# Kernel tuning notes

Hardware: AMD Instinct MI355X
Metric: run time of the kernel (lower is better)

Reference implementation:

```python
import jax, jax.numpy as jnp
import numpy as np

T = 2048       # tokens (flattened, single causal sequence)
HID = 2048     # hidden_size
H = 16         # num_heads
DN = 128       # qk_nope_head_dim
DR = 64        # qk_rope_head_dim
DV = 128       # v_head_dim
DQK = DN + DR  # 192
QLR = 1536     # q_lora_rank
KVLR = 512     # kv_lora_rank
THETA = 10000.0
EPS = 1e-6
SCALE = DQK ** -0.5


def rmsnorm(x, w):
    return x * jax.lax.rsqrt(jnp.mean(x * x, axis=-1, keepdims=True) + EPS) * w


def rope_interleaved(x, cos, sin):
    # is_neox_style=False: rotate interleaved even/odd pairs
    x1 = x[..., 0::2]
    x2 = x[..., 1::2]
    out = jnp.stack([x1 * cos - x2 * sin, x2 * cos + x1 * sin], axis=-1)
    return out.reshape(x.shape)


def setup_inputs() -> dict:
    key = jax.random.key(0)
    ks = jax.random.split(key, 8)
    s = 0.02
    return {
        "positions": jnp.arange(T, dtype=jnp.int32),
        "hidden_states": jax.random.normal(ks[0], (T, HID), jnp.float32),
        "w_q_a": jax.random.normal(ks[1], (HID, QLR), jnp.float32) * s,
        "q_a_ln_w": jnp.ones((QLR,), jnp.float32),
        "w_q_b": jax.random.normal(ks[2], (QLR, H * DQK), jnp.float32) * s,
        "w_kv_a": jax.random.normal(ks[3], (HID, KVLR + DR), jnp.float32) * s,
        "kv_a_ln_w": jnp.ones((KVLR,), jnp.float32),
        "w_kv_b": jax.random.normal(ks[4], (KVLR, H * (DN + DV)), jnp.float32) * s,
        "w_o": jax.random.normal(ks[5], (H * DV, HID), jnp.float32) * s,
    }


def reference(positions, hidden_states, w_q_a, q_a_ln_w, w_q_b, w_kv_a,
              kv_a_ln_w, w_kv_b, w_o):
    t = hidden_states.shape[0]
    # --- Q low-rank path ---
    q = rmsnorm(hidden_states @ w_q_a, q_a_ln_w) @ w_q_b          # [T, H*DQK]
    q = q.reshape(t, H, DQK)
    q_nope, q_pe = q[..., :DN], q[..., DN:]
    # --- KV latent path ---
    latent = hidden_states @ w_kv_a                                # [T, KVLR+DR]
    kv_a = rmsnorm(latent[:, :KVLR], kv_a_ln_w)
    kv = (kv_a @ w_kv_b).reshape(t, H, DN + DV)
    k_nope, v = kv[..., :DN], kv[..., DN:]
    k_pe = latent[:, None, KVLR:]                                  # [T, 1, DR]
    # --- partial RoPE (non-neox, interleaved) ---
    inv_freq = 1.0 / (THETA ** (jnp.arange(0, DR, 2, dtype=jnp.float32) / DR))
    ang = positions.astype(jnp.float32)[:, None] * inv_freq        # [T, DR/2]
    cos = jnp.cos(ang)[:, None, :]
    sin = jnp.sin(ang)[:, None, :]
    q_pe = rope_interleaved(q_pe, cos, sin)
    k_pe = rope_interleaved(k_pe, cos, sin)
    q = jnp.concatenate([q_nope, q_pe], axis=-1)                   # [T, H, DQK]
    k = jnp.concatenate([k_nope, jnp.broadcast_to(k_pe, (t, H, DR))], axis=-1)
    # --- causal attention (V zero-padded to DQK then sliced == using V directly) ---
    scores = jnp.einsum("thd,shd->hts", q, k) * SCALE              # [H, T, T]
    causal = positions[None, :, None] >= positions[None, None, :]
    scores = jnp.where(causal, scores, jnp.finfo(scores.dtype).min)
    probs = jax.nn.softmax(scores, axis=-1)
    attn = jnp.einsum("hts,shd->thd", probs, v)                    # [T, H, DV]
    return attn.reshape(t, H * DV) @ w_o                           # [T, HID]
```

## Files before the change

kernel.cpp:

```cpp
#include <hip/hip_runtime.h>
#include <hip/hip_bf16.h>

#define T_ 2048
#define SCALE_ 0.07216878364870322f

typedef __bf16 bf16x8 __attribute__((ext_vector_type(8)));
typedef float f32x4 __attribute__((ext_vector_type(4)));
typedef float f32x16 __attribute__((ext_vector_type(16)));

__device__ inline bf16x8 load8f(const float* p) {
    const float4* f = reinterpret_cast<const float4*>(p);
    float4 a = f[0], b = f[1];
    bf16x8 r;
    r[0] = (__bf16)a.x; r[1] = (__bf16)a.y; r[2] = (__bf16)a.z; r[3] = (__bf16)a.w;
    r[4] = (__bf16)b.x; r[5] = (__bf16)b.y; r[6] = (__bf16)b.z; r[7] = (__bf16)b.w;
    return r;
}

__device__ inline void gld_lds16(const void* g, void* l) {
    __builtin_amdgcn_global_load_lds((const __attribute__((address_space(1))) void*)g,
                                     (__attribute__((address_space(3))) void*)l, 16, 0, 0);
}

__global__ __launch_bounds__(256) void cvt_bf16(const float* __restrict__ in,
                                                __bf16* __restrict__ out, int n8)
{
    int i = blockIdx.x * 256 + threadIdx.x;
    if (i < n8)
        *reinterpret_cast<bf16x8*>(out + (size_t)i * 8) = load8f(in + (size_t)i * 8);
}

__global__ __launch_bounds__(256) void transpose_cvt(
    const float* __restrict__ W, __bf16* __restrict__ Wt, int K, int N)
{
    __shared__ __bf16 tl[64][72];
    const int k0 = blockIdx.x * 64, n0 = blockIdx.y * 64;
    const int tid = threadIdx.x;
    const bool in = n0 < N;
    #pragma unroll
    for (int it = 0; it < 2; ++it) {
        int chunk = tid + it * 256;
        int r = chunk >> 3;
        int c8 = (chunk & 7) * 8;
        float4 a = {0,0,0,0}, b = {0,0,0,0};
        if (in) {
            const float* p = W + (size_t)(k0 + r) * N + n0 + c8;
            a = *reinterpret_cast<const float4*>(p);
            b = *reinterpret_cast<const float4*>(p + 4);
        }
        tl[c8+0][r] = (__bf16)a.x; tl[c8+1][r] = (__bf16)a.y;
        tl[c8+2][r] = (__bf16)a.z; tl[c8+3][r] = (__bf16)a.w;
        tl[c8+4][r] = (__bf16)b.x; tl[c8+5][r] = (__bf16)b.y;
        tl[c8+6][r] = (__bf16)b.z; tl[c8+7][r] = (__bf16)b.w;
    }
    __syncthreads();
    #pragma unroll
    for (int it = 0; it < 2; ++it) {
        int chunk = tid + it * 256;
        int n = chunk >> 3;
        int k8 = (chunk & 7) * 8;
        bf16x8 v = *reinterpret_cast<const bf16x8*>(&tl[n][k8]);
        *reinterpret_cast<bf16x8*>(Wt + (size_t)(n0 + n) * K + k0 + k8) = v;
    }
}

template <typename TC>
__device__ __forceinline__ void gemm_body(
    const __bf16* __restrict__ A, const __bf16* __restrict__ Bt,
    TC* __restrict__ C, int K, int Nstore, int ldc, int m0, int n0,
    __bf16* As, __bf16* Bs)
{
    const int tid = threadIdx.x, lane = tid & 63, wid = tid >> 6;
    const int l15 = lane & 15, lg = lane >> 4;
    const int wr = (wid >> 1) * 64, wc = (wid & 1) * 64;

    const int srow = wid * 32 + (lane >> 3);
    const int scol = ((lane & 7) ^ (lane >> 3)) * 8;
    const __bf16* Ag = A  + (size_t)(m0 + srow) * K + scol;
    const __bf16* Bg = Bt + (size_t)(n0 + srow) * K + scol;
    const int lbase = wid * 4096;

    f32x4 acc[4][4] = {};

    {
        char* la = (char*)As + lbase;
        char* lb = (char*)Bs + lbase;
        #pragma unroll
        for (int i = 0; i < 4; ++i) {
            gld_lds16(Ag + (size_t)i * 8 * K, la + i * 1024);
            gld_lds16(Bg + (size_t)i * 8 * K, lb + i * 1024);
        }
    }
    __syncthreads();

    int cur = 0;
    for (int k0 = 0; k0 < K; k0 += 64) {
        if (k0 + 64 < K) {
            char* la = (char*)As + (cur ^ 1) * 16384 + lbase;
            char* lb = (char*)Bs + (cur ^ 1) * 16384 + lbase;
            #pragma unroll
            for (int i = 0; i < 4; ++i) {
                gld_lds16(Ag + (size_t)i * 8 * K + k0 + 64, la + i * 1024);
                gld_lds16(Bg + (size_t)i * 8 * K + k0 + 64, lb + i * 1024);
            }
        }

        bf16x8 af[4][2], bf[4][2];
        #pragma unroll
        for (int i = 0; i < 4; ++i) {
            const int Ra = wr + i * 16 + l15;
            const int Rb = wc + i * 16 + l15;
            const int ca = (lg ^ (Ra & 7)) * 16;
            const int cb = (lg ^ (Rb & 7)) * 16;
            const char* pa = (const char*)As + cur * 16384 + Ra * 128;
            const char* pb = (const char*)Bs + cur * 16384 + Rb * 128;
            af[i][0] = *reinterpret_cast<const bf16x8*>(pa + ca);
            af[i][1] = *reinterpret_cast<const bf16x8*>(pa + (ca ^ 64));
            bf[i][0] = *reinterpret_cast<const bf16x8*>(pb + cb);
            bf[i][1] = *reinterpret_cast<const bf16x8*>(pb + (cb ^ 64));
        }
        #pragma unroll
        for (int h = 0; h < 2; ++h)
            #pragma unroll
            for (int i = 0; i < 4; ++i)
                #pragma unroll
                for (int j = 0; j < 4; ++j)
                    acc[i][j] = __builtin_amdgcn_mfma_f32_16x16x32_bf16(af[i][h], bf[j][h], acc[i][j], 0, 0, 0);

        __syncthreads();
        cur ^= 1;
    }

    #pragma unroll
    for (int i = 0; i < 4; ++i)
        #pragma unroll
        for (int j = 0; j < 4; ++j)
            #pragma unroll
            for (int e = 0; e < 4; ++e) {
                int r = m0 + wr + i * 16 + lg * 4 + e;
                int c = n0 + wc + j * 16 + l15;
                if (c < Nstore)
                    C[(size_t)r * ldc + c] = (TC)acc[i][j][e];
            }
}

template <typename TC>
__global__ __launch_bounds__(256) void gemm_bt(
    const __bf16* __restrict__ A, const __bf16* __restrict__ Bt,
    TC* __restrict__ C, int M, int N, int K, int Nstore, int ldc)
{
    __shared__ __bf16 As[2 * 128 * 64];
    __shared__ __bf16 Bs[2 * 128 * 64];
    gemm_body<TC>(A, Bt, C, K, Nstore, ldc, blockIdx.x * 128, blockIdx.y * 128, As, Bs);
}

__global__ __launch_bounds__(256) void gemm_bt_pair(
    const __bf16* __restrict__ A0, const __bf16* __restrict__ B0, __bf16* __restrict__ C0,
    int N0, int K0, int nby0,
    const __bf16* __restrict__ A1, const __bf16* __restrict__ B1, __bf16* __restrict__ C1,
    int N1, int K1)
{
    __shared__ __bf16 As[2 * 128 * 64];
    __shared__ __bf16 Bs[2 * 128 * 64];
    if ((int)blockIdx.y < nby0)
        gemm_body<__bf16>(A0, B0, C0, K0, N0, N0, blockIdx.x * 128, blockIdx.y * 128, As, Bs);
    else
        gemm_body<__bf16>(A1, B1, C1, K1, N1, N1, blockIdx.x * 128, (blockIdx.y - nby0) * 128, As, Bs);
}

__global__ __launch_bounds__(256) void rmsnorm_fused(
    const __bf16* __restrict__ qkv_a,
    const float* __restrict__ qw, const float* __restrict__ kw,
    __bf16* __restrict__ q_a_n, __bf16* __restrict__ kv_a_n)
{
    const int t = blockIdx.x, tid = threadIdx.x, wid = tid >> 6;
    const bool isq = tid < 192;
    const __bf16* src = qkv_a + (size_t)t * 2176 + (isq ? tid * 8 : 1536 + (tid - 192) * 8);
    float x[8];
    float ss = 0.f;
    bf16x8 v = *reinterpret_cast<const bf16x8*>(src);
    #pragma unroll
    for (int e = 0; e < 8; ++e) { x[e] = (float)v[e]; ss += x[e] * x[e]; }
    #pragma unroll
    for (int m = 1; m < 64; m <<= 1) ss += __shfl_xor(ss, m, 64);
    __shared__ float red[4];
    if ((tid & 63) == 0) red[wid] = ss;
    __syncthreads();
    float scale;
    const float* w;
    if (isq) {
        scale = rsqrtf((red[0] + red[1] + red[2]) / 1536.f + 1e-6f);
        w = qw + tid * 8;
    } else {
        scale = rsqrtf(red[3] / 512.f + 1e-6f);
        w = kw + (tid - 192) * 8;
    }
    float4 w0 = *reinterpret_cast<const float4*>(w);
    float4 w1 = *reinterpret_cast<const float4*>(w + 4);
    bf16x8 o;
    o[0] = (__bf16)(x[0] * scale * w0.x); o[1] = (__bf16)(x[1] * scale * w0.y);
    o[2] = (__bf16)(x[2] * scale * w0.z); o[3] = (__bf16)(x[3] * scale * w0.w);
    o[4] = (__bf16)(x[4] * scale * w1.x); o[5] = (__bf16)(x[5] * scale * w1.y);
    o[6] = (__bf16)(x[6] * scale * w1.z); o[7] = (__bf16)(x[7] * scale * w1.w);
    if (isq)
        *reinterpret_cast<bf16x8*>(q_a_n + (size_t)t * 1536 + tid * 8) = o;
    else
        *reinterpret_cast<bf16x8*>(kv_a_n + (size_t)t * 512 + (tid - 192) * 8) = o;
}

__global__ __launch_bounds__(256) void rope_kprep(
    const int* __restrict__ positions, __bf16* __restrict__ q,
    const __bf16* __restrict__ kv, const __bf16* __restrict__ qkv_a,
    __bf16* __restrict__ kh)
{
    const int t = blockIdx.x, tid = threadIdx.x;
    __shared__ float cs[32], sn[32];
    __shared__ __bf16 kpe[64];
    if (tid < 32) {
        float pos = (float)positions[t];
        float invf = powf(10000.f, -(float)tid / 32.f);
        float c = cosf(pos * invf), s = sinf(pos * invf);
        cs[tid] = c; sn[tid] = s;
        float x1 = (float)qkv_a[(size_t)t * 2176 + 2048 + 2 * tid];
        float x2 = (float)qkv_a[(size_t)t * 2176 + 2049 + 2 * tid];
        kpe[2 * tid]     = (__bf16)(x1 * c - x2 * s);
        kpe[2 * tid + 1] = (__bf16)(x2 * c + x1 * s);
    }
    __syncthreads();
    #pragma unroll
    for (int it = 0; it < 2; ++it) {
        int p = tid + it * 256;
        int h = p >> 5, i = p & 31;
        size_t base = (size_t)t * 3072 + h * 192 + 128 + 2 * i;
        float x1 = (float)q[base], x2 = (float)q[base + 1];
        q[base]     = (__bf16)(x1 * cs[i] - x2 * sn[i]);
        q[base + 1] = (__bf16)(x2 * cs[i] + x1 * sn[i]);
    }
    const int h = tid >> 4, c = tid & 15;
    const int sw = t & 7;
    bf16x8 v = *reinterpret_cast<const bf16x8*>(kv + (size_t)t * 4096 + h * 256 + c * 8);
    *reinterpret_cast<bf16x8*>(kh + ((size_t)h * T_ + t) * 192 + (c ^ sw) * 8) = v;
    if (c < 8) {
        bf16x8 p = *reinterpret_cast<const bf16x8*>(&kpe[c * 8]);
        *reinterpret_cast<bf16x8*>(kh + ((size_t)h * T_ + t) * 192 + 128 + (c ^ sw) * 8) = p;
    }
}

__global__ __launch_bounds__(256) void vtrans(
    const __bf16* __restrict__ kv, __bf16* __restrict__ vt)
{
    __shared__ __bf16 tile[128][72];
    const int t0 = blockIdx.x * 64;
    const int h  = blockIdx.y;
    const int tid = threadIdx.x;
    #pragma unroll
    for (int it = 0; it < 4; ++it) {
        int chunk = tid + it * 256;
        int r = chunk >> 4;
        int d8 = (chunk & 15) * 8;
        bf16x8 v = *reinterpret_cast<const bf16x8*>(kv + (size_t)(t0 + r) * 4096 + h * 256 + 128 + d8);
        #pragma unroll
        for (int e = 0; e < 8; ++e) tile[d8 + e][r] = v[e];
    }
    __syncthreads();
    #pragma unroll
    for (int it = 0; it < 4; ++it) {
        int chunk = tid + it * 256;
        int d = chunk >> 3;
        int t8 = (chunk & 7) * 8;
        bf16x8 v = *reinterpret_cast<const bf16x8*>(&tile[d][t8]);
        *reinterpret_cast<bf16x8*>(vt + ((size_t)h * 128 + d) * 2048 + t0 + t8) = v;
    }
}

__device__ inline unsigned pk2(float a, float b) {
    union { __bf16 h[2]; unsigned u; } z;
    z.h[0] = (__bf16)a; z.h[1] = (__bf16)b;
    return z.u;
}

union AttnSmem {
    char kstage[4][12288];
    struct {
        float mls[2][4][32];
        float linv[32];
        float obuf[32][129];
    } c;
};

__global__ __launch_bounds__(256, 2) void attn_flash(
    const __bf16* __restrict__ q, const __bf16* __restrict__ kh,
    const __bf16* __restrict__ vt, __bf16* __restrict__ attn)
{
    __shared__ AttnSmem sm;
    const int tid = threadIdx.x;
    const int lane = tid & 63, wid = tid >> 6;
    const int q31 = lane & 31, hi = lane >> 5;
    const int b = blockIdx.x;
    const int h = b & 15;
    const int qt = 63 - (b >> 4);
    const int q0 = qt * 32;
    const int ntile = qt + 1;

    const __bf16* Khh = kh + (size_t)h * T_ * 192;
    const __bf16* Vt  = vt + (size_t)h * 128 * T_;
    const __bf16* Qp  = q + (size_t)(q0 + q31) * 3072 + h * 192;

    bf16x8 aq[12];
    #pragma unroll
    for (int c = 0; c < 12; ++c)
        aq[c] = *reinterpret_cast<const bf16x8*>(Qp + c * 16 + hi * 8);

    f32x16 o[4] = {};
    float m_i = -1e30f, l_i = 0.f;

    char* kbuf = sm.kstage[wid];

    if (wid < ntile) {
        const __bf16* src = Khh + (size_t)(wid * 32) * 192 + lane * 8;
        #pragma unroll
        for (int i = 0; i < 12; ++i)
            gld_lds16(src + i * 512, kbuf + i * 1024);
    }

    for (int it = wid; it < ntile; it += 4) {
        asm volatile("s_waitcnt vmcnt(0)" ::: "memory");
        __builtin_amdgcn_sched_barrier(0);

        bf16x8 kc[12];
        #pragma unroll
        for (int c = 0; c < 12; ++c) {
            const int p = (2 * c + hi) ^ (q31 & 7);
            kc[c] = *reinterpret_cast<const bf16x8*>(kbuf + q31 * 384 + p * 16);
        }
        asm volatile("s_waitcnt lgkmcnt(0)" ::: "memory");
        __builtin_amdgcn_sched_barrier(0);

        const bool notlast = (it + 4 < ntile);
        if (notlast) {
            const __bf16* src = Khh + (size_t)((it + 4) * 32) * 192 + lane * 8;
            #pragma unroll
            for (int i = 0; i < 12; ++i)
                gld_lds16(src + i * 512, kbuf + i * 1024);
        }

        const int s0 = it * 32;
        bf16x8 vf[4][2];
        #pragma unroll
        for (int n = 0; n < 4; ++n)
            #pragma unroll
            for (int m = 0; m < 2; ++m)
                vf[n][m] = *reinterpret_cast<const bf16x8*>(
                    Vt + (size_t)(n * 32 + q31) * 2048 + s0 + (2 * m + hi) * 8);

        f32x16 sA = {}, sB = {};
        __builtin_amdgcn_s_setprio(1);
        #pragma unroll
        for (int c = 0; c < 12; c += 2) {
            sA = __builtin_amdgcn_mfma_f32_32x32x16_bf16(kc[c],     aq[c],     sA, 0, 0, 0);
            sB = __builtin_amdgcn_mfma_f32_32x32x16_bf16(kc[c + 1], aq[c + 1], sB, 0, 0, 0);
        }
        __builtin_amdgcn_s_setprio(0);

        float v[16];
        #pragma unroll
        for (int r = 0; r < 16; ++r) v[r] = (sA[r] + sB[r]) * SCALE_;
        if (it == qt) {
            #pragma unroll
            for (int r = 0; r < 16; ++r) {
                int crow = (r & 3) + 8 * (r >> 2) + 4 * hi;
                if (crow > q31) v[r] = -1e30f;
            }
        }
        float mx = v[0];
        #pragma unroll
        for (int r = 1; r < 16; ++r) mx = fmaxf(mx, v[r]);
        mx = fmaxf(mx, __shfl_xor(mx, 32, 64));
        const bool skip = __all(mx <= m_i);
        float mnew = fmaxf(m_i, mx);
        float fsc = skip ? 1.f : __expf(m_i - mnew);
        m_i = mnew;
        float ps = 0.f;
        #pragma unroll
        for (int r = 0; r < 16; ++r) { v[r] = __expf(v[r] - mnew); ps += v[r]; }
        ps += __shfl_xor(ps, 32, 64);
        l_i = l_i * fsc + ps;
        if (!skip) {
            #pragma unroll
            for (int n = 0; n < 4; ++n) o[n] *= fsc;
        }

        unsigned w[8], xw[8];
        #pragma unroll
        for (int i = 0; i < 8; ++i) w[i] = pk2(v[2 * i], v[2 * i + 1]);
        #pragma unroll
        for (int i = 0; i < 8; ++i) xw[i] = __shfl_xor(w[i], 32, 64);
        union { unsigned u[4]; bf16x8 v; } P0, P1;
        P0.u[0] = hi ? xw[2] : w[0]; P0.u[1] = hi ? xw[3] : w[1];
        P0.u[2] = hi ? w[2] : xw[0]; P0.u[3] = hi ? w[3] : xw[1];
        P1.u[0] = hi ? xw[6] : w[4]; P1.u[1] = hi ? xw[7] : w[5];
        P1.u[2] = hi ? w[6] : xw[4]; P1.u[3] = hi ? w[7] : xw[5];

        __builtin_amdgcn_s_setprio(1);
        #pragma unroll
        for (int n = 0; n < 4; ++n) {
            o[n] = __builtin_amdgcn_mfma_f32_32x32x16_bf16(vf[n][0], P0.v, o[n], 0, 0, 0);
            o[n] = __builtin_amdgcn_mfma_f32_32x32x16_bf16(vf[n][1], P1.v, o[n], 0, 0, 0);
        }
        __builtin_amdgcn_s_setprio(0);
    }

    __syncthreads();
    if (hi == 0) { sm.c.mls[0][wid][q31] = m_i; sm.c.mls[1][wid][q31] = l_i; }
    __syncthreads();
    float M = fmaxf(fmaxf(sm.c.mls[0][0][q31], sm.c.mls[0][1][q31]),
                    fmaxf(sm.c.mls[0][2][q31], sm.c.mls[0][3][q31]));
    float L = sm.c.mls[1][0][q31] * __expf(sm.c.mls[0][0][q31] - M)
            + sm.c.mls[1][1][q31] * __expf(sm.c.mls[0][1][q31] - M)
            + sm.c.mls[1][2][q31] * __expf(sm.c.mls[0][2][q31] - M)
            + sm.c.mls[1][3][q31] * __expf(sm.c.mls[0][3][q31] - M);
    float F = __expf(m_i - M);
    if (wid == 0 && hi == 0) sm.c.linv[q31] = 1.f / L;

    #pragma unroll
    for (int rd = 0; rd < 4; ++rd) {
        if (wid == rd) {
            if (rd == 0) {
                #pragma unroll
                for (int n = 0; n < 4; ++n)
                    #pragma unroll
                    for (int r = 0; r < 16; ++r) {
                        int d = (r & 3) + 8 * (r >> 2) + 4 * hi + 32 * n;
                        sm.c.obuf[q31][d] = F * o[n][r];
                    }
            } else {
                #pragma unroll
                for (int n = 0; n < 4; ++n)
                    #pragma unroll
                    for (int r = 0; r < 16; ++r) {
                        int d = (r & 3) + 8 * (r >> 2) + 4 * hi + 32 * n;
                        sm.c.obuf[q31][d] += F * o[n][r];
                    }
            }
        }
        __syncthreads();
    }

    #pragma unroll
    for (int it2 = 0; it2 < 2; ++it2) {
        int cidx = tid + it2 * 256;
        int row = cidx >> 4, c8 = (cidx & 15) * 8;
        float inv = sm.c.linv[row];
        bf16x8 vv;
        #pragma unroll
        for (int j = 0; j < 8; ++j)
            vv[j] = (__bf16)(sm.c.obuf[row][c8 + j] * inv);
        *reinterpret_cast<bf16x8*>(attn + (size_t)(q0 + row) * 2048 + h * 128 + c8) = vv;
    }
}

extern "C" void kernel_launch(void* const* d_in, const int* in_sizes, int n_in,
                              void* d_out, int out_size, void* d_ws, size_t ws_size,
                              hipStream_t stream)
{
    const int*   positions = (const int*)d_in[0];
    const float* hidden    = (const float*)d_in[1];
    const float* w_q_a     = (const float*)d_in[2];
    const float* q_a_ln_w  = (const float*)d_in[3];
    const float* w_q_b     = (const float*)d_in[4];
    const float* w_kv_a    = (const float*)d_in[5];
    const float* kv_a_ln_w = (const float*)d_in[6];
    const float* w_kv_b    = (const float*)d_in[7];
    const float* w_o       = (const float*)d_in[8];

    char* ws = (char*)d_ws;
    __bf16* hidden_bf = (__bf16*)(ws);
    __bf16* vt        = (__bf16*)(ws);
    __bf16* wbuf      = (__bf16*)(ws + 8388608);
    __bf16* qkv_a     = (__bf16*)(ws + 17825792);
    __bf16* attn      = (__bf16*)(ws + 17825792);
    __bf16* q_a_n     = (__bf16*)(ws + 26738688);
    __bf16* q         = (__bf16*)(ws + 33030144);
    __bf16* kv_a_n    = (__bf16*)(ws + 45613056);
    __bf16* kv        = (__bf16*)(ws + 47710208);
    __bf16* kh        = (__bf16*)(ws + 64487424);
    __bf16* wbuf2     = (__bf16*)(ws + 77070336);

    dim3 blk(256);
    cvt_bf16<<<dim3(2048), blk, 0, stream>>>(hidden, hidden_bf, 524288);

    transpose_cvt<<<dim3(32, 24), blk, 0, stream>>>(w_q_a, wbuf, 2048, 1536);
    transpose_cvt<<<dim3(32, 10), blk, 0, stream>>>(w_kv_a, wbuf + (size_t)1536 * 2048, 2048, 576);
    gemm_bt<__bf16><<<dim3(16, 17), blk, 0, stream>>>(hidden_bf, wbuf, qkv_a, 2048, 2176, 2048, 2112, 2176);
    rmsnorm_fused<<<dim3(2048), blk, 0, stream>>>(qkv_a, q_a_ln_w, kv_a_ln_w, q_a_n, kv_a_n);

    transpose_cvt<<<dim3(24, 48), blk, 0, stream>>>(w_q_b, wbuf, 1536, 3072);
    transpose_cvt<<<dim3(8, 64), blk, 0, stream>>>(w_kv_b, wbuf2, 512, 4096);
    gemm_bt_pair<<<dim3(16, 56), blk, 0, stream>>>(
        q_a_n, wbuf, q, 3072, 1536, 24,
        kv_a_n, wbuf2, kv, 4096, 512);

    rope_kprep<<<dim3(2048), blk, 0, stream>>>(positions, q, kv, qkv_a, kh);
    vtrans<<<dim3(32, 16), blk, 0, stream>>>(kv, vt);
    attn_flash<<<dim3(1024), dim3(256), 0, stream>>>(q, kh, vt, attn);

    transpose_cvt<<<dim3(32, 32), blk, 0, stream>>>(w_o, wbuf, 2048, 2048);
    gemm_bt<float><<<dim3(16, 16), blk, 0, stream>>>(attn, wbuf, (float*)d_out, 2048, 2048, 2048, 2048, 2048);
}
```

Measured before the change: 221.8 us.

## Process two K tiles per attention loop iteration with direct global K loads

Each wave now handles two key tiles per loop trip, tile it through the LDS-staged buffer and tile it+4 through direct global register loads of K issued before the first QK MFMA. The LDS prefetch now targets it+8. The aim is more memory-level parallelism and better latency hiding between the two tiles' loads and MFMAs. It costs more registers (a second K fragment and V fragment set), which may lower occupancy, and the second tile's K reads bypass LDS. The direct loads apply a swizzle based on the row index, which only matches the data if the K buffer in global memory is itself stored swizzled.

```diff
diff --git a/kernel.cpp b/kernel.cpp
--- a/kernel.cpp
+++ b/kernel.cpp
@@ -323,7 +323,10 @@
             gld_lds16(src + i * 512, kbuf + i * 1024);
     }
 
-    for (int it = wid; it < ntile; it += 4) {
+    for (int it = wid; it < ntile; it += 8) {
+        const int itB = it + 4;
+        const bool hasB = (itB < ntile);
+
         asm volatile("s_waitcnt vmcnt(0)" ::: "memory");
         __builtin_amdgcn_sched_barrier(0);
 
@@ -336,14 +339,6 @@
         asm volatile("s_waitcnt lgkmcnt(0)" ::: "memory");
         __builtin_amdgcn_sched_barrier(0);
 
-        const bool notlast = (it + 4 < ntile);
-        if (notlast) {
-            const __bf16* src = Khh + (size_t)((it + 4) * 32) * 192 + lane * 8;
-            #pragma unroll
-            for (int i = 0; i < 12; ++i)
-                gld_lds16(src + i * 512, kbuf + i * 1024);
-        }
-
         const int s0 = it * 32;
         bf16x8 vf[4][2];
         #pragma unroll
@@ -353,6 +348,24 @@
                 vf[n][m] = *reinterpret_cast<const bf16x8*>(
                     Vt + (size_t)(n * 32 + q31) * 2048 + s0 + (2 * m + hi) * 8);
 
+        if (it + 8 < ntile) {
+            const __bf16* src = Khh + (size_t)((it + 8) * 32) * 192 + lane * 8;
+            #pragma unroll
+            for (int i = 0; i < 12; ++i)
+                gld_lds16(src + i * 512, kbuf + i * 1024);
+        }
+
+        bf16x8 kb[12];
+        if (hasB) {
+            const __bf16* KgB = Khh + (size_t)(itB * 32 + q31) * 192;
+            const int swB = (itB * 32 + q31) & 7;
+            #pragma unroll
+            for (int c = 0; c < 12; ++c) {
+                const int p = (2 * c + hi) ^ swB;
+                kb[c] = *reinterpret_cast<const bf16x8*>(KgB + p * 8);
+            }
+        }
+
         f32x16 sA = {}, sB = {};
         __builtin_amdgcn_s_setprio(1);
         #pragma unroll
@@ -362,52 +375,121 @@
         }
         __builtin_amdgcn_s_setprio(0);
 
-        float v[16];
-        #pragma unroll
-        for (int r = 0; r < 16; ++r) v[r] = (sA[r] + sB[r]) * SCALE_;
-        if (it == qt) {
-            #pragma unroll
-            for (int r = 0; r < 16; ++r) {
-                int crow = (r & 3) + 8 * (r >> 2) + 4 * hi;
-                if (crow > q31) v[r] = -1e30f;
-            }
-        }
-        float mx = v[0];
-        #pragma unroll
-        for (int r = 1; r < 16; ++r) mx = fmaxf(mx, v[r]);
-        mx = fmaxf(mx, __shfl_xor(mx, 32, 64));
-        const bool skip = __all(mx <= m_i);
-        float mnew = fmaxf(m_i, mx);
-        float fsc = skip ? 1.f : __expf(m_i - mnew);
-        m_i = mnew;
-        float ps = 0.f;
-        #pragma unroll
-        for (int r = 0; r < 16; ++r) { v[r] = __expf(v[r] - mnew); ps += v[r]; }
-        ps += __shfl_xor(ps, 32, 64);
-        l_i = l_i * fsc + ps;
-        if (!skip) {
-            #pragma unroll
-            for (int n = 0; n < 4; ++n) o[n] *= fsc;
-        }
-
-        unsigned w[8], xw[8];
-        #pragma unroll
-        for (int i = 0; i < 8; ++i) w[i] = pk2(v[2 * i], v[2 * i + 1]);
-        #pragma unroll
-        for (int i = 0; i < 8; ++i) xw[i] = __shfl_xor(w[i], 32, 64);
-        union { unsigned u[4]; bf16x8 v; } P0, P1;
-        P0.u[0] = hi ? xw[2] : w[0]; P0.u[1] = hi ? xw[3] : w[1];
-        P0.u[2] = hi ? w[2] : xw[0]; P0.u[3] = hi ? w[3] : xw[1];
-        P1.u[0] = hi ? xw[6] : w[4]; P1.u[1] = hi ? xw[7] : w[5];
-        P1.u[2] = hi ? w[6] : xw[4]; P1.u[3] = hi ? w[7] : xw[5];
-
-        __builtin_amdgcn_s_setprio(1);
-        #pragma unroll
-        for (int n = 0; n < 4; ++n) {
-            o[n] = __builtin_amdgcn_mfma_f32_32x32x16_bf16(vf[n][0], P0.v, o[n], 0, 0, 0);
-            o[n] = __builtin_amdgcn_mfma_f32_32x32x16_bf16(vf[n][1], P1.v, o[n], 0, 0, 0);
-        }
-        __builtin_amdgcn_s_setprio(0);
+        {
+            float v[16];
+            #pragma unroll
+            for (int r = 0; r < 16; ++r) v[r] = (sA[r] + sB[r]) * SCALE_;
+            if (it == qt) {
+                #pragma unroll
+                for (int r = 0; r < 16; ++r) {
+                    int crow = (r & 3) + 8 * (r >> 2) + 4 * hi;
+                    if (crow > q31) v[r] = -1e30f;
+                }
+            }
+            float mx = v[0];
+            #pragma unroll
+            for (int r = 1; r < 16; ++r) mx = fmaxf(mx, v[r]);
+            mx = fmaxf(mx, __shfl_xor(mx, 32, 64));
+            const bool skip = __all(mx <= m_i);
+            float mnew = fmaxf(m_i, mx);
+            float fsc = skip ? 1.f : __expf(m_i - mnew);
+            m_i = mnew;
+            float ps = 0.f;
+            #pragma unroll
+            for (int r = 0; r < 16; ++r) { v[r] = __expf(v[r] - mnew); ps += v[r]; }
+            ps += __shfl_xor(ps, 32, 64);
+            l_i = l_i * fsc + ps;
+            if (!skip) {
+                #pragma unroll
+                for (int n = 0; n < 4; ++n) o[n] *= fsc;
+            }
+
+            unsigned w[8], xw[8];
+            #pragma unroll
+            for (int i = 0; i < 8; ++i) w[i] = pk2(v[2 * i], v[2 * i + 1]);
+            #pragma unroll
+            for (int i = 0; i < 8; ++i) xw[i] = __shfl_xor(w[i], 32, 64);
+            union { unsigned u[4]; bf16x8 v; } P0, P1;
+            P0.u[0] = hi ? xw[2] : w[0]; P0.u[1] = hi ? xw[3] : w[1];
+            P0.u[2] = hi ? w[2] : xw[0]; P0.u[3] = hi ? w[3] : xw[1];
+            P1.u[0] = hi ? xw[6] : w[4]; P1.u[1] = hi ? xw[7] : w[5];
+            P1.u[2] = hi ? w[6] : xw[4]; P1.u[3] = hi ? w[7] : xw[5];
+
+            __builtin_amdgcn_s_setprio(1);
+            #pragma unroll
+            for (int n = 0; n < 4; ++n) {
+                o[n] = __builtin_amdgcn_mfma_f32_32x32x16_bf16(vf[n][0], P0.v, o[n], 0, 0, 0);
+                o[n] = __builtin_amdgcn_mfma_f32_32x32x16_bf16(vf[n][1], P1.v, o[n], 0, 0, 0);
+            }
+            __builtin_amdgcn_s_setprio(0);
+        }
+
+        if (hasB) {
+            const int s0B = itB * 32;
+            bf16x8 vfB[4][2];
+            #pragma unroll
+            for (int n = 0; n < 4; ++n)
+                #pragma unroll
+                for (int m = 0; m < 2; ++m)
+                    vfB[n][m] = *reinterpret_cast<const bf16x8*>(
+                        Vt + (size_t)(n * 32 + q31) * 2048 + s0B + (2 * m + hi) * 8);
+
+            f32x16 tA = {}, tB = {};
+            __builtin_amdgcn_s_setprio(1);
+            #pragma unroll
+            for (int c = 0; c < 12; c += 2) {
+                tA = __builtin_amdgcn_mfma_f32_32x32x16_bf16(kb[c],     aq[c],     tA, 0, 0, 0);
+                tB = __builtin_amdgcn_mfma_f32_32x32x16_bf16(kb[c + 1], aq[c + 1], tB, 0, 0, 0);
+            }
+            __builtin_amdgcn_s_setprio(0);
+
+            float v[16];
+            #pragma unroll
+            for (int r = 0; r < 16; ++r) v[r] = (tA[r] + tB[r]) * SCALE_;
+            if (itB == qt) {
+                #pragma unroll
+                for (int r = 0; r < 16; ++r) {
+                    int crow = (r & 3) + 8 * (r >> 2) + 4 * hi;
+                    if (crow > q31) v[r] = -1e30f;
+                }
+            }
+            float mx = v[0];
+            #pragma unroll
+            for (int r = 1; r < 16; ++r) mx = fmaxf(mx, v[r]);
+            mx = fmaxf(mx, __shfl_xor(mx, 32, 64));
+            const bool skip = __all(mx <= m_i);
+            float mnew = fmaxf(m_i, mx);
+            float fsc = skip ? 1.f : __expf(m_i - mnew);
+            m_i = mnew;
+            float ps = 0.f;
+            #pragma unroll
+            for (int r = 0; r < 16; ++r) { v[r] = __expf(v[r] - mnew); ps += v[r]; }
+            ps += __shfl_xor(ps, 32, 64);
+            l_i = l_i * fsc + ps;
+            if (!skip) {
+                #pragma unroll
+                for (int n = 0; n < 4; ++n) o[n] *= fsc;
+            }
+
+            unsigned w[8], xw[8];
+            #pragma unroll
+            for (int i = 0; i < 8; ++i) w[i] = pk2(v[2 * i], v[2 * i + 1]);
+            #pragma unroll
+            for (int i = 0; i < 8; ++i) xw[i] = __shfl_xor(w[i], 32, 64);
+            union { unsigned u[4]; bf16x8 v; } P0, P1;
+            P0.u[0] = hi ? xw[2] : w[0]; P0.u[1] = hi ? xw[3] : w[1];
+            P0.u[2] = hi ? w[2] : xw[0]; P0.u[3] = hi ? w[3] : xw[1];
+            P1.u[0] = hi ? xw[6] : w[4]; P1.u[1] = hi ? xw[7] : w[5];
+            P1.u[2] = hi ? w[6] : xw[4]; P1.u[3] = hi ? w[7] : xw[5];
+
+            __builtin_amdgcn_s_setprio(1);
+            #pragma unroll
+            for (int n = 0; n < 4; ++n) {
+                o[n] = __builtin_amdgcn_mfma_f32_32x32x16_bf16(vfB[n][0], P0.v, o[n], 0, 0, 0);
+                o[n] = __builtin_amdgcn_mfma_f32_32x32x16_bf16(vfB[n][1], P1.v, o[n], 0, 0, 0);
+            }
+            __builtin_amdgcn_s_setprio(0);
+        }
     }
 
     __syncthreads();
```

Result: slower. 289.1 us (+30.3%).
